# Performance work log

Hardware: AMD Instinct MI355X
Metric: run time of the kernel (lower is better)

Reference implementation:

```python
import jax, jax.numpy as jnp
import numpy as np

D = 2048      # hidden dim
H = 16        # heads
BSZ = 4       # batch
L = 2048      # seq len
BASE_DT = 0.1


def setup_inputs() -> dict:
    key = jax.random.key(0)
    ks = jax.random.split(key, 9)
    s = 1.0 / np.sqrt(D)
    x = jax.random.normal(ks[0], (BSZ, L, D), dtype=jnp.float32)
    v = jax.random.normal(ks[1], (BSZ, L, D), dtype=jnp.float32)
    force = jax.random.normal(ks[2], (BSZ, L, D), dtype=jnp.float32)
    WA = jax.random.normal(ks[3], (D, D), dtype=jnp.float32) * s
    bA = jnp.zeros((D,), dtype=jnp.float32)
    WB = jax.random.normal(ks[4], (D, D), dtype=jnp.float32) * s
    bB = jnp.zeros((D,), dtype=jnp.float32)
    Wdt = jax.random.normal(ks[5], (D, D), dtype=jnp.float32) * s
    bdt = jnp.zeros((D,), dtype=jnp.float32)
    # base_dt_scales buffer: 1.5**head_index, repeated head_dim times
    scales = jnp.repeat(1.5 ** jnp.arange(H, dtype=jnp.float32), D // H)
    return {"x": x, "v": v, "force": force, "WA": WA, "bA": bA,
            "WB": WB, "bB": bB, "Wdt": Wdt, "bdt": bdt, "scales": scales}


def _combine(e1, e2):
    # associative op for v_t = a_t * v_{t-1} + b_t ; e1 is the earlier element
    a1, b1 = e1
    a2, b2 = e2
    return a1 * a2, a2 * b1 + b2


def reference(x, v, force, WA, bA, WB, bB, Wdt, bdt, scales):
    # x is LayerNorm-ed in the original but the result is unused; v is unused.
    A = jax.nn.sigmoid(force @ WA + bA)                      # [B, L, D] in (0,1)
    dt = jax.nn.softplus(force @ Wdt + bdt) * BASE_DT * scales  # per-head dt scaling
    B_val = (force @ WB + bB) * dt
    # parallel associative scan over the sequence axis: v_t = A_t v_{t-1} + B_t
    _, v_seq = jax.lax.associative_scan(_combine, (A, B_val), axis=1)
    # second scan has A=1 -> plain prefix sum
    x_seq = jnp.cumsum(v_seq * dt, axis=1)
    return x_seq, v_seq
```

## Files before the change

kernel.cpp:

```cpp
#include <hip/hip_runtime.h>
#include <hip/hip_bf16.h>
#include <cstdint>
#include <cstddef>

#define D_DIM 2048
#define L_SEQ 2048
#define B_SZ 4
#define M_ROWS (B_SZ * L_SEQ)
#define NT_COLS (3 * D_DIM)
#define NCH 16
#define CHUNK (L_SEQ / NCH)

typedef __bf16 bf16_t;
typedef bf16_t bf16x8 __attribute__((ext_vector_type(8)));
typedef float f32x4 __attribute__((ext_vector_type(4)));

__device__ __forceinline__ void gl_lds16(const void* g, void* l) {
    __builtin_amdgcn_global_load_lds(
        (const __attribute__((address_space(1))) unsigned int*)g,
        (__attribute__((address_space(3))) unsigned int*)l, 16, 0, 0);
}

#define BAR()    asm volatile("s_barrier" ::: "memory")
#define VMCNT8() asm volatile("s_waitcnt vmcnt(8)" ::: "memory")
#define VMCNT0() asm volatile("s_waitcnt vmcnt(0)" ::: "memory")

__global__ __launch_bounds__(256) void cvt_bf16_kernel(
    const float* __restrict__ in, bf16_t* __restrict__ out, int n8)
{
    int i = blockIdx.x * 256 + threadIdx.x;
    if (i >= n8) return;
    float4 f0 = ((const float4*)in)[2 * i];
    float4 f1 = ((const float4*)in)[2 * i + 1];
    bf16x8 o;
    o[0] = (bf16_t)f0.x; o[1] = (bf16_t)f0.y; o[2] = (bf16_t)f0.z; o[3] = (bf16_t)f0.w;
    o[4] = (bf16_t)f1.x; o[5] = (bf16_t)f1.y; o[6] = (bf16_t)f1.z; o[7] = (bf16_t)f1.w;
    ((bf16x8*)out)[i] = o;
}

__global__ __launch_bounds__(256) void transpose_w_kernel(
    const float* __restrict__ W0, const float* __restrict__ W1,
    const float* __restrict__ W2, bf16_t* __restrict__ Wt)
{
    __shared__ float tile[32][33];
    const float* W = (blockIdx.z == 0) ? W0 : (blockIdx.z == 1) ? W1 : W2;
    bf16_t* dst = Wt + (size_t)blockIdx.z * D_DIM * D_DIM;
    int j0 = blockIdx.x * 32, k0 = blockIdx.y * 32;
    int tx = threadIdx.x, ty = threadIdx.y;
#pragma unroll
    for (int i = 0; i < 4; i++) {
        int k = k0 + ty + i * 8;
        tile[ty + i * 8][tx] = W[(size_t)k * D_DIM + j0 + tx];
    }
    __syncthreads();
#pragma unroll
    for (int i = 0; i < 4; i++) {
        int j = j0 + ty + i * 8;
        dst[(size_t)j * D_DIM + k0 + tx] = (bf16_t)tile[tx][ty + i * 8];
    }
}

#define STAGE(LA, LB, T) {                                                     \
    const size_t kofs_ = (size_t)(T) * 32;                                     \
    gl_lds16(gA0 + kofs_, (LA) + w * 512);                                     \
    gl_lds16(gA1 + kofs_, (LA) + 2048 + w * 512);                              \
    gl_lds16(gB0 + kofs_, (LB) + w * 512);                                     \
    gl_lds16(gB1 + kofs_, (LB) + 2048 + w * 512);                              \
}

#define COMPUTE(LA, LB) {                                                      \
    bf16x8 af[4], bfr[4];                                                      \
    _Pragma("unroll") for (int m = 0; m < 4; m++)                              \
        af[m] = *(const bf16x8*)&(LA)[(wr + m * 16) * 32 + lof];               \
    _Pragma("unroll") for (int n = 0; n < 4; n++)                              \
        bfr[n] = *(const bf16x8*)&(LB)[(wc + n * 16) * 32 + lof];              \
    __builtin_amdgcn_s_setprio(1);                                             \
    _Pragma("unroll") for (int m = 0; m < 4; m++)                              \
        _Pragma("unroll") for (int n = 0; n < 4; n++)                          \
            acc[m][n] = __builtin_amdgcn_mfma_f32_16x16x32_bf16(               \
                af[m], bfr[n], acc[m][n], 0, 0, 0);                            \
    __builtin_amdgcn_s_setprio(0);                                             \
}

#define PHASE(BUFA, BUFB, T, DSTA, DSTB) {                                     \
    STAGE(DSTA, DSTB, (T) + 2);                                                \
    COMPUTE(BUFA, BUFB);                                                       \
    VMCNT8();                                                                  \
    BAR();                                                                     \
}

__global__ __launch_bounds__(256) void gemm_fused_kernel(
    const bf16_t* __restrict__ Abf,
    const bf16_t* __restrict__ Wt,
    const float* __restrict__ bA, const float* __restrict__ bdt,
    const float* __restrict__ bB, const float* __restrict__ scales,
    float* __restrict__ outA,
    float* __restrict__ outDT,
    float* __restrict__ outB)
{
    __shared__ bf16_t lds_a[3][128 * 32];
    __shared__ bf16_t lds_b[3][128 * 32];

    const int bm0 = blockIdx.x * 128;
    const int bn0 = blockIdx.y * 128;
    const int t = threadIdx.x;
    const int lane = t & 63, w = t >> 6;
    const int wr = (w >> 1) * 64;
    const int wc = (w & 1) * 64;

    f32x4 acc[4][4] = {};

    const int ar0 = t >> 2;
    const int ac0 = (((t & 3) ^ ((t >> 3) & 3)) << 3);
    const bf16_t* gA0 = Abf + (size_t)(bm0 + ar0) * D_DIM + ac0;
    const bf16_t* gA1 = Abf + (size_t)(bm0 + ar0 + 64) * D_DIM + ac0;
    const bf16_t* gB0 = Wt + (size_t)(bn0 + ar0) * D_DIM + ac0;
    const bf16_t* gB1 = Wt + (size_t)(bn0 + ar0 + 64) * D_DIM + ac0;

    const int frow = lane & 15;
    const int lof = frow * 32 + (((lane >> 4) ^ ((frow >> 1) & 3)) << 3);

    STAGE(lds_a[0], lds_b[0], 0);
    STAGE(lds_a[1], lds_b[1], 1);
    VMCNT8();
    BAR();

#pragma unroll 1
    for (int i = 0; i < 20; ++i) {
        const int t3 = 3 * i;
        PHASE(lds_a[0], lds_b[0], t3,     lds_a[2], lds_b[2]);
        PHASE(lds_a[1], lds_b[1], t3 + 1, lds_a[0], lds_b[0]);
        PHASE(lds_a[2], lds_b[2], t3 + 2, lds_a[1], lds_b[1]);
    }
    PHASE(lds_a[0], lds_b[0], 60, lds_a[2], lds_b[2]);
    PHASE(lds_a[1], lds_b[1], 61, lds_a[0], lds_b[0]);
    COMPUTE(lds_a[2], lds_b[2]);
    VMCNT0();
    BAR();
    COMPUTE(lds_a[0], lds_b[0]);

    const int seg = bn0 >> 11;
    const int dbase = (bn0 & 2047) + wc + (lane & 15);
    const int rowbase = bm0 + wr + ((lane >> 4) << 2);

    if (seg == 0) {
        float bias[4];
#pragma unroll
        for (int n = 0; n < 4; n++) bias[n] = bA[dbase + n * 16];
#pragma unroll
        for (int m = 0; m < 4; m++)
#pragma unroll
            for (int n = 0; n < 4; n++)
#pragma unroll
                for (int r = 0; r < 4; r++) {
                    size_t idx = (size_t)(rowbase + m * 16 + r) * D_DIM + dbase + n * 16;
                    outA[idx] = 1.0f / (1.0f + __expf(-(acc[m][n][r] + bias[n])));
                }
    } else if (seg == 1) {
        float bias[4], sc[4];
#pragma unroll
        for (int n = 0; n < 4; n++) { bias[n] = bdt[dbase + n * 16]; sc[n] = scales[dbase + n * 16]; }
#pragma unroll
        for (int m = 0; m < 4; m++)
#pragma unroll
            for (int n = 0; n < 4; n++)
#pragma unroll
                for (int r = 0; r < 4; r++) {
                    size_t idx = (size_t)(rowbase + m * 16 + r) * D_DIM + dbase + n * 16;
                    float xx = acc[m][n][r] + bias[n];
                    float sp = xx > 0.f ? xx + log1pf(__expf(-xx)) : log1pf(__expf(xx));
                    outDT[idx] = sp * 0.1f * sc[n];
                }
    } else {
        float bias[4];
#pragma unroll
        for (int n = 0; n < 4; n++) bias[n] = bB[dbase + n * 16];
#pragma unroll
        for (int m = 0; m < 4; m++)
#pragma unroll
            for (int n = 0; n < 4; n++)
#pragma unroll
                for (int r = 0; r < 4; r++) {
                    size_t idx = (size_t)(rowbase + m * 16 + r) * D_DIM + dbase + n * 16;
                    outB[idx] = acc[m][n][r] + bias[n];
                }
    }
}

__global__ __launch_bounds__(256) void scan_pass1_kernel(
    const float* __restrict__ Aarr, const float* __restrict__ Braw,
    const float* __restrict__ dtv, float4* __restrict__ agg)
{
    int pp = blockIdx.x * 256 + threadIdx.x;
    int dp = (pp & 1023) << 1;
    int c = (pp >> 10) & (NCH - 1);
    int b = pp >> 14;
    size_t base = ((size_t)(b * L_SEQ + c * CHUNK)) * D_DIM + dp;
    float P0 = 1.f, R0 = 0.f, U0 = 0.f, W0 = 0.f;
    float P1 = 1.f, R1 = 0.f, U1 = 0.f, W1 = 0.f;
#pragma unroll 4
    for (int tt = 0; tt < CHUNK; tt++) {
        size_t idx = base + (size_t)tt * D_DIM;
        float2 a2  = *(const float2*)&Aarr[idx];
        float2 rb2 = *(const float2*)&Braw[idx];
        float2 dt2 = *(const float2*)&dtv[idx];
        float bv0 = rb2.x * dt2.x, bv1 = rb2.y * dt2.y;
        float da0 = dt2.x * a2.x,  da1 = dt2.y * a2.y;
        R0 = da0 * P0 + R0;  W0 = da0 * U0 + dt2.x * bv0 + W0;
        U0 = a2.x * U0 + bv0;  P0 = a2.x * P0;
        R1 = da1 * P1 + R1;  W1 = da1 * U1 + dt2.y * bv1 + W1;
        U1 = a2.y * U1 + bv1;  P1 = a2.y * P1;
    }
    int ch = ((b * NCH + c) << 11) + dp;
    agg[ch]     = make_float4(P0, R0, U0, W0);
    agg[ch + 1] = make_float4(P1, R1, U1, W1);
}

__global__ __launch_bounds__(256) void scan_pass2_kernel(
    const float4* __restrict__ agg, float2* __restrict__ pre)
{
    int tid = blockIdx.x * 256 + threadIdx.x;
    int d = tid & (D_DIM - 1);
    int b = tid >> 11;
    float v = 0.f, x = 0.f;
#pragma unroll
    for (int c = 0; c < NCH; c++) {
        int i = ((b * NCH + c) << 11) + d;
        float4 g = agg[i];
        pre[i] = make_float2(v, x);
        float vn = g.x * v + g.z;
        x = g.y * v + x + g.w;
        v = vn;
    }
}

__global__ __launch_bounds__(256) void scan_pass3_kernel(
    const float* __restrict__ dtv, const float2* __restrict__ pre,
    float* __restrict__ xout, float* __restrict__ vout)
{
    int pp = blockIdx.x * 256 + threadIdx.x;
    int dp = (pp & 1023) << 1;
    int c = (pp >> 10) & (NCH - 1);
    int b = pp >> 14;
    int ch = ((b * NCH + c) << 11) + dp;
    float4 pv = *(const float4*)&pre[ch];
    float v0 = pv.x, x0 = pv.y, v1 = pv.z, x1 = pv.w;
    size_t base = ((size_t)(b * L_SEQ + c * CHUNK)) * D_DIM + dp;
#pragma unroll 4
    for (int tt = 0; tt < CHUNK; tt++) {
        size_t idx = base + (size_t)tt * D_DIM;
        float2 a2  = *(const float2*)&xout[idx];
        float2 rb2 = *(const float2*)&vout[idx];
        float2 dt2 = *(const float2*)&dtv[idx];
        v0 = a2.x * v0 + rb2.x * dt2.x;
        x0 = x0 + v0 * dt2.x;
        v1 = a2.y * v1 + rb2.y * dt2.y;
        x1 = x1 + v1 * dt2.y;
        *(float2*)&vout[idx] = make_float2(v0, v1);
        *(float2*)&xout[idx] = make_float2(x0, x1);
    }
}

extern "C" void kernel_launch(void* const* d_in, const int* in_sizes, int n_in,
                              void* d_out, int out_size, void* d_ws, size_t ws_size,
                              hipStream_t stream) {
    const float* force  = (const float*)d_in[2];
    const float* WA     = (const float*)d_in[3];
    const float* bA     = (const float*)d_in[4];
    const float* WB     = (const float*)d_in[5];
    const float* bB     = (const float*)d_in[6];
    const float* Wdt    = (const float*)d_in[7];
    const float* bdt    = (const float*)d_in[8];
    const float* scales = (const float*)d_in[9];

    float* xout = (float*)d_out;
    float* vout = xout + (size_t)M_ROWS * D_DIM;

    char* ws = (char*)d_ws;
    bf16_t* fbf = (bf16_t*)ws;
    bf16_t* wt  = (bf16_t*)(ws + (size_t)33554432);
    float*  dtv = (float*)(ws + (size_t)33554432 + 25165824);
    float4* agg = (float4*)(ws + (size_t)33554432 + 25165824 + 67108864);
    float2* pre = (float2*)(ws + (size_t)33554432 + 25165824 + 67108864 + 2097152);

    {
        int n8 = M_ROWS * D_DIM / 8;
        cvt_bf16_kernel<<<n8 / 256, 256, 0, stream>>>(force, fbf, n8);
    }
    {
        dim3 grid(D_DIM / 32, D_DIM / 32, 3), block(32, 8);
        transpose_w_kernel<<<grid, block, 0, stream>>>(WA, Wdt, WB, wt);
    }
    {
        dim3 grid(M_ROWS / 128, NT_COLS / 128);
        gemm_fused_kernel<<<grid, 256, 0, stream>>>(fbf, wt, bA, bdt, bB, scales,
                                                    xout, dtv, vout);
    }
    scan_pass1_kernel<<<(B_SZ * NCH * D_DIM / 2) / 256, 256, 0, stream>>>(xout, vout, dtv, agg);
    scan_pass2_kernel<<<(B_SZ * D_DIM) / 256, 256, 0, stream>>>(agg, pre);
    scan_pass3_kernel<<<(B_SZ * NCH * D_DIM / 2) / 256, 256, 0, stream>>>(dtv, pre, xout, vout);
}
```

Measured before the change: 474.0 us.

## Enlarge GEMM block tile to 256x128 with 8 waves and double buffering

The fused GEMM block tile grows from 128x128 with 4 waves to 256x128 with 8 waves, so each staged weight tile is reused across twice as many rows. The LDS pipeline drops from three buffers with a partial vmcnt wait to two buffers with a full vmcnt(0) wait each step. Launch bounds are set to 512 threads with 4 blocks per CU, which tightens the per-thread register budget while the 64-float accumulator stays the same. The aim is less global and LDS traffic per FLOP, at the risk of register spills and less overlap of loads with compute.

```diff
diff --git a/kernel.cpp b/kernel.cpp
--- a/kernel.cpp
+++ b/kernel.cpp
@@ -22,7 +22,6 @@
 }
 
 #define BAR()    asm volatile("s_barrier" ::: "memory")
-#define VMCNT8() asm volatile("s_waitcnt vmcnt(8)" ::: "memory")
 #define VMCNT0() asm volatile("s_waitcnt vmcnt(0)" ::: "memory")
 
 __global__ __launch_bounds__(256) void cvt_bf16_kernel(
@@ -63,9 +62,8 @@
 #define STAGE(LA, LB, T) {                                                     \
     const size_t kofs_ = (size_t)(T) * 32;                                     \
     gl_lds16(gA0 + kofs_, (LA) + w * 512);                                     \
-    gl_lds16(gA1 + kofs_, (LA) + 2048 + w * 512);                              \
+    gl_lds16(gA1 + kofs_, (LA) + 4096 + w * 512);                              \
     gl_lds16(gB0 + kofs_, (LB) + w * 512);                                     \
-    gl_lds16(gB1 + kofs_, (LB) + 2048 + w * 512);                              \
 }
 
 #define COMPUTE(LA, LB) {                                                      \
@@ -82,14 +80,7 @@
     __builtin_amdgcn_s_setprio(0);                                             \
 }
 
-#define PHASE(BUFA, BUFB, T, DSTA, DSTB) {                                     \
-    STAGE(DSTA, DSTB, (T) + 2);                                                \
-    COMPUTE(BUFA, BUFB);                                                       \
-    VMCNT8();                                                                  \
-    BAR();                                                                     \
-}
-
-__global__ __launch_bounds__(256) void gemm_fused_kernel(
+__global__ __launch_bounds__(512, 4) void gemm_fused_kernel(
     const bf16_t* __restrict__ Abf,
     const bf16_t* __restrict__ Wt,
     const float* __restrict__ bA, const float* __restrict__ bdt,
@@ -98,10 +89,12 @@
     float* __restrict__ outDT,
     float* __restrict__ outB)
 {
-    __shared__ bf16_t lds_a[3][128 * 32];
-    __shared__ bf16_t lds_b[3][128 * 32];
-
-    const int bm0 = blockIdx.x * 128;
+    __shared__ bf16_t lds_a0[256 * 32];
+    __shared__ bf16_t lds_a1[256 * 32];
+    __shared__ bf16_t lds_b0[128 * 32];
+    __shared__ bf16_t lds_b1[128 * 32];
+
+    const int bm0 = blockIdx.x * 256;
     const int bn0 = blockIdx.y * 128;
     const int t = threadIdx.x;
     const int lane = t & 63, w = t >> 6;
@@ -110,38 +103,41 @@
 
     f32x4 acc[4][4] = {};
 
-    const int ar0 = t >> 2;
-    const int ac0 = (((t & 3) ^ ((t >> 3) & 3)) << 3);
-    const bf16_t* gA0 = Abf + (size_t)(bm0 + ar0) * D_DIM + ac0;
-    const bf16_t* gA1 = Abf + (size_t)(bm0 + ar0 + 64) * D_DIM + ac0;
-    const bf16_t* gB0 = Wt + (size_t)(bn0 + ar0) * D_DIM + ac0;
-    const bf16_t* gB1 = Wt + (size_t)(bn0 + ar0 + 64) * D_DIM + ac0;
+    const int srow = t >> 2;
+    const int scol = (((t & 3) ^ ((t >> 3) & 3)) << 3);
+    const bf16_t* gA0 = Abf + (size_t)(bm0 + srow) * D_DIM + scol;
+    const bf16_t* gA1 = Abf + (size_t)(bm0 + 128 + srow) * D_DIM + scol;
+    const bf16_t* gB0 = Wt + (size_t)(bn0 + srow) * D_DIM + scol;
 
     const int frow = lane & 15;
-    const int lof = frow * 32 + (((lane >> 4) ^ ((frow >> 1) & 3)) << 3);
-
-    STAGE(lds_a[0], lds_b[0], 0);
-    STAGE(lds_a[1], lds_b[1], 1);
-    VMCNT8();
-    BAR();
-
-#pragma unroll 1
-    for (int i = 0; i < 20; ++i) {
-        const int t3 = 3 * i;
-        PHASE(lds_a[0], lds_b[0], t3,     lds_a[2], lds_b[2]);
-        PHASE(lds_a[1], lds_b[1], t3 + 1, lds_a[0], lds_b[0]);
-        PHASE(lds_a[2], lds_b[2], t3 + 2, lds_a[1], lds_b[1]);
-    }
-    PHASE(lds_a[0], lds_b[0], 60, lds_a[2], lds_b[2]);
-    PHASE(lds_a[1], lds_b[1], 61, lds_a[0], lds_b[0]);
-    COMPUTE(lds_a[2], lds_b[2]);
+    const int q = lane >> 4;
+    const int lof = frow * 32 + (((q) ^ ((frow >> 1) & 3)) << 3);
+
+    STAGE(lds_a0, lds_b0, 0);
     VMCNT0();
     BAR();
-    COMPUTE(lds_a[0], lds_b[0]);
+
+#pragma unroll 1
+    for (int i = 0; i < 31; ++i) {
+        const int tt = 2 * i;
+        STAGE(lds_a1, lds_b1, tt + 1);
+        COMPUTE(lds_a0, lds_b0);
+        VMCNT0();
+        BAR();
+        STAGE(lds_a0, lds_b0, tt + 2);
+        COMPUTE(lds_a1, lds_b1);
+        VMCNT0();
+        BAR();
+    }
+    STAGE(lds_a1, lds_b1, 63);
+    COMPUTE(lds_a0, lds_b0);
+    VMCNT0();
+    BAR();
+    COMPUTE(lds_a1, lds_b1);
 
     const int seg = bn0 >> 11;
     const int dbase = (bn0 & 2047) + wc + (lane & 15);
-    const int rowbase = bm0 + wr + ((lane >> 4) << 2);
+    const int rowbase = bm0 + wr + (q << 2);
 
     if (seg == 0) {
         float bias[4];
@@ -292,8 +288,8 @@
         transpose_w_kernel<<<grid, block, 0, stream>>>(WA, Wdt, WB, wt);
     }
     {
-        dim3 grid(M_ROWS / 128, NT_COLS / 128);
-        gemm_fused_kernel<<<grid, 256, 0, stream>>>(fbf, wt, bA, bdt, bB, scales,
+        dim3 grid(M_ROWS / 256, NT_COLS / 128);
+        gemm_fused_kernel<<<grid, 512, 0, stream>>>(fbf, wt, bA, bdt, bB, scales,
                                                     xout, dtv, vout);
     }
     scan_pass1_kernel<<<(B_SZ * NCH * D_DIM / 2) / 256, 256, 0, stream>>>(xout, vout, dtv, agg);
```

Measured after the change: 414.1 us. 12.6% less time.
